# Performance work log

Hardware: AMD Instinct MI355X
Metric: run time of the kernel (lower is better)

## Reference

```python
import jax, jax.numpy as jnp
import numpy as np

B, S, H, E, F, TOP_K = 4, 2048, 512, 16, 1024, 2


def setup_inputs() -> dict:
    key = jax.random.key(0)
    k0, k1, k2, k3, k4 = jax.random.split(key, 5)
    scale = 0.02
    return {
        "inputs": jax.random.normal(k0, (B, S, H), dtype=jnp.float32),
        "router_w": jax.random.normal(k1, (E, H), dtype=jnp.float32) * scale,
        "gate_w": jax.random.normal(k2, (E, H, F), dtype=jnp.float32) * scale,
        "up_w": jax.random.normal(k3, (E, H, F), dtype=jnp.float32) * scale,
        "down_w": jax.random.normal(k4, (E, F, H), dtype=jnp.float32) * scale,
    }


def _moe_forward(inputs, router_w, gate_w, up_w, down_w):
    b, s, h = inputs.shape
    x = inputs.reshape(-1, h)                      # [T, H]
    T = x.shape[0]
    # --- routing: topk of logits then fp32 softmax over the k selected ---
    router_logits = x @ router_w.T                 # [T, E]
    top_vals, top_idx = jax.lax.top_k(router_logits, TOP_K)   # [T, K]
    weights = jax.nn.softmax(top_vals.astype(jnp.float32), axis=-1)  # [T, K]
    # dense combine weights: w[t, e] = routing weight if expert e selected else 0
    combine = jnp.zeros((T, router_w.shape[0]), jnp.float32)
    combine = combine.at[jnp.arange(T)[:, None], top_idx].set(weights)  # [T, E]

    # --- per-expert SwiGLU MLP, weighted combine (scan over experts) ---
    def step(acc, ew):
        wg, wu, wd, ce = ew                        # [H,F], [H,F], [F,H], [T]
        hid = jax.nn.silu(x @ wg) * (x @ wu)       # [T, F]
        y = hid @ wd                               # [T, H]
        return acc + ce[:, None] * y, None

    out0 = jnp.zeros_like(x)
    out, _ = jax.lax.scan(step, out0, (gate_w, up_w, down_w, combine.T))
    return out.reshape(b, s, h), router_logits, top_idx


def reference(inputs, router_w, gate_w, up_w, down_w):
    out, router_logits, selected_experts = _moe_forward(
        inputs, router_w, gate_w, up_w, down_w)
    return out
```

## Files before the change

kernel.cpp:

```cpp
#include <hip/hip_runtime.h>
#include <cstdint>
#include <cstddef>

#define T_TOK 8192
#define H_DIM 512
#define E_NUM 16
#define F_DIM 1024

typedef __bf16 bf16x8 __attribute__((ext_vector_type(8)));
typedef float f32x4 __attribute__((ext_vector_type(4)));

#define OFF_XBF  0UL
#define OFF_HID  8388608UL
#define OFF_GW   41943040UL
#define OFF_UW   58720256UL
#define OFF_DW   75497472UL
#define OFF_STOK 92274688UL
#define OFF_SW   92340224UL
#define OFF_TOPE 92405760UL
#define OFF_TOPW 92471296UL
#define OFF_CNT  92536832UL
#define OFF_CUR  92537856UL
#define OFF_OFFS 92538880UL
#define OFF_SIDX 92539904UL
#define OFF_L128 92605440UL
#define OFF_L64  92606464UL
#define OFF_YB   OFF_GW

__device__ __forceinline__ unsigned short f2bf(float f) {
  union { float f; uint32_t u; } v; v.f = f;
  uint32_t r = v.u + 0x7fffu + ((v.u >> 16) & 1u);
  return (unsigned short)(r >> 16);
}

__device__ __forceinline__ float bf2f(unsigned short u) {
  union { uint32_t u; float f; } v; v.u = (uint32_t)u << 16;
  return v.f;
}

__device__ __forceinline__ void gld16(const void* g, void* l) {
  __builtin_amdgcn_global_load_lds(
      (const __attribute__((address_space(1))) unsigned int*)g,
      (__attribute__((address_space(3))) unsigned int*)l, 16, 0, 0);
}

__global__ __launch_bounds__(256) void k_pre(
    const float* __restrict__ x, const float* __restrict__ rw,
    const float* __restrict__ gw, const float* __restrict__ uw,
    const float* __restrict__ dw,
    unsigned short* __restrict__ xbf, int* __restrict__ tope,
    float* __restrict__ topw,
    unsigned short* __restrict__ gws, unsigned short* __restrict__ uws,
    unsigned short* __restrict__ dws) {
  const int bid = blockIdx.x;
  const int tid = threadIdx.x;
  __shared__ __align__(16) uint32_t lsu[4096];

  if (bid < 3072) {
    const int isgu = (bid < 2048);
    const float* src;
    unsigned short* dst;
    size_t obase0;
    int ldn;
    int e, kc;
    if (isgu) {
      e = bid >> 7;
      const int mat = (bid >> 6) & 1;
      kc = (bid >> 2) & 15;
      const int f2 = bid & 3;
      src = (mat ? uw : gw) + (size_t)e * H_DIM * F_DIM + (size_t)kc * 32 * F_DIM + f2 * 256;
      dst = mat ? uws : gws;
      obase0 = (((size_t)e * 8 + f2 * 2) * 16 + kc) * 4096;
      ldn = F_DIM;
    } else {
      const int r = bid - 2048;
      e = r >> 6;
      kc = (r >> 1) & 31;
      const int ht = r & 1;
      src = dw + (size_t)e * F_DIM * H_DIM + (size_t)kc * 32 * H_DIM + ht * 256;
      dst = dws;
      obase0 = (((size_t)e * 2 + ht) * 32 + kc) * 8192;
      ldn = H_DIM;
    }
    const int nb = tid & 63, kb = tid >> 6;
    const float* s0 = src + (size_t)kb * 8 * ldn + nb * 4;
    float4 v[8];
    #pragma unroll
    for (int j = 0; j < 8; ++j) v[j] = *(const float4*)(s0 + (size_t)j * ldn);
    #pragma unroll
    for (int i = 0; i < 4; ++i) {
      const int n = nb * 4 + i;
      uint4 q;
      q.x = (uint32_t)f2bf(((const float*)&v[0])[i]) | ((uint32_t)f2bf(((const float*)&v[1])[i]) << 16);
      q.y = (uint32_t)f2bf(((const float*)&v[2])[i]) | ((uint32_t)f2bf(((const float*)&v[3])[i]) << 16);
      q.z = (uint32_t)f2bf(((const float*)&v[4])[i]) | ((uint32_t)f2bf(((const float*)&v[5])[i]) << 16);
      q.w = (uint32_t)f2bf(((const float*)&v[6])[i]) | ((uint32_t)f2bf(((const float*)&v[7])[i]) << 16);
      const int jr = n >> 1, sw = (jr ^ (jr >> 3)) & 7;
      const int ccs = (((n & 1) << 2) + kb) ^ sw;
      *(uint4*)&lsu[jr * 32 + ccs * 4] = q;
    }
    __syncthreads();
    const int n = tid;
    const int jr = n >> 1, sw = (jr ^ (jr >> 3)) & 7;
    #pragma unroll
    for (int c = 0; c < 4; ++c) {
      const int ccs = (((n & 1) << 2) + c) ^ sw;
      uint4 q = *(const uint4*)&lsu[jr * 32 + ccs * 4];
      if (isgu) {
        const int fi = n & 127, s = (c ^ fi) & 3;
        const size_t ob = obase0 + (size_t)(n >> 7) * 16 * 4096;
        *(uint4*)&dst[ob + fi * 32 + s * 8] = q;
      } else {
        const int s = (c ^ n) & 3;
        *(uint4*)&dst[obase0 + n * 32 + s * 8] = q;
      }
    }
  } else {
    const int rb = bid - 3072;
    const int wave = tid >> 6, lane = tid & 63;
    const int t = rb * 4 + wave;
    const float4* xr = (const float4*)(x + (size_t)t * H_DIM + lane * 8);
    float4 a = xr[0], b = xr[1];
    float xi[8] = {a.x, a.y, a.z, a.w, b.x, b.y, b.z, b.w};
    uint4 o;
    o.x = (uint32_t)f2bf(xi[0]) | ((uint32_t)f2bf(xi[1]) << 16);
    o.y = (uint32_t)f2bf(xi[2]) | ((uint32_t)f2bf(xi[3]) << 16);
    o.z = (uint32_t)f2bf(xi[4]) | ((uint32_t)f2bf(xi[5]) << 16);
    o.w = (uint32_t)f2bf(xi[6]) | ((uint32_t)f2bf(xi[7]) << 16);
    *(uint4*)(xbf + (size_t)t * H_DIM + lane * 8) = o;
    float acc[E_NUM];
    #pragma unroll
    for (int e = 0; e < E_NUM; ++e) {
      const float4* wr = (const float4*)(rw + e * H_DIM + lane * 8);
      float4 wa = wr[0], wb = wr[1];
      acc[e] = xi[0]*wa.x + xi[1]*wa.y + xi[2]*wa.z + xi[3]*wa.w
             + xi[4]*wb.x + xi[5]*wb.y + xi[6]*wb.z + xi[7]*wb.w;
    }
    #pragma unroll
    for (int off = 1; off < 64; off <<= 1) {
      #pragma unroll
      for (int e = 0; e < E_NUM; ++e) acc[e] += __shfl_xor(acc[e], off);
    }
    if (lane == 0) {
      int e0 = 0; float v0 = acc[0];
      #pragma unroll
      for (int e = 1; e < E_NUM; ++e) if (acc[e] > v0) { v0 = acc[e]; e0 = e; }
      int e1 = -1; float v1 = -3.4e38f;
      #pragma unroll
      for (int e = 0; e < E_NUM; ++e) if (e != e0 && acc[e] > v1) { v1 = acc[e]; e1 = e; }
      float ee = __expf(v1 - v0);
      float inv = 1.0f / (1.0f + ee);
      tope[t*2]   = e0; tope[t*2+1] = e1;
      topw[t*2]   = inv; topw[t*2+1] = ee * inv;
    }
  }
}

__global__ __launch_bounds__(256) void k_hist(
    const int* __restrict__ tope, int* __restrict__ counts) {
  __shared__ int lh[E_NUM];
  const int tid = threadIdx.x;
  if (tid < E_NUM) lh[tid] = 0;
  __syncthreads();
  atomicAdd(&lh[tope[blockIdx.x * 256 + tid]], 1);
  __syncthreads();
  if (tid < E_NUM) atomicAdd(&counts[tid * 16], lh[tid]);
}

__global__ void k_offsets(const int* __restrict__ counts, int* __restrict__ offs,
                          int* __restrict__ list128, int* __restrict__ list64) {
  __shared__ int sc[16], b128[16], b64[16];
  if (threadIdx.x == 0) {
    int s = 0, a = 0, b = 0;
    for (int e = 0; e < E_NUM; ++e) {
      int c = counts[e * 16];
      sc[e] = c; b128[e] = a; b64[e] = b;
      offs[e] = s;
      s += c; a += (c + 127) >> 7; b += (c + 63) >> 6;
    }
    offs[16] = s; offs[18] = a; offs[19] = b;
  }
  __syncthreads();
  for (int e = 0; e < E_NUM; ++e) {
    const int n1 = (sc[e] + 127) >> 7;
    for (int ti = threadIdx.x; ti < n1; ti += 64) list128[b128[e] + ti] = (e << 24) | (ti << 7);
    const int n2 = (sc[e] + 63) >> 6;
    for (int ti = threadIdx.x; ti < n2; ti += 64) list64[b64[e] + ti] = (e << 24) | (ti << 6);
  }
}

__global__ __launch_bounds__(256) void k_scatter(
    const int* __restrict__ tope, const float* __restrict__ topw,
    const int* __restrict__ offs, int* __restrict__ cursors,
    int* __restrict__ stok, float* __restrict__ sw, int* __restrict__ sidx) {
  __shared__ int lh[E_NUM];
  __shared__ int lbase[E_NUM];
  const int tid = threadIdx.x;
  const int t = blockIdx.x * 256 + tid;
  if (tid < E_NUM) lh[tid] = 0;
  __syncthreads();
  int e0 = tope[t*2], e1 = tope[t*2+1];
  int r0 = atomicAdd(&lh[e0], 1);
  int r1 = atomicAdd(&lh[e1], 1);
  __syncthreads();
  if (tid < E_NUM) lbase[tid] = atomicAdd(&cursors[tid * 16], lh[tid]);
  __syncthreads();
  int s0 = offs[e0] + lbase[e0] + r0;
  int s1 = offs[e1] + lbase[e1] + r1;
  stok[s0] = t; sw[s0] = topw[t*2];
  stok[s1] = t; sw[s1] = topw[t*2+1];
  sidx[t*2] = s0; sidx[t*2+1] = s1;
}

__global__ __launch_bounds__(256, 2) void k_gateup(
    const unsigned short* __restrict__ xbf,
    const unsigned short* __restrict__ gws, const unsigned short* __restrict__ uws,
    const int* __restrict__ stok, const int* __restrict__ counts,
    const int* __restrict__ offs, const int* __restrict__ list128,
    unsigned short* __restrict__ hid) {
  const int y = blockIdx.y;
  if (y >= offs[18]) return;
  const int v = list128[y];
  const int e = v >> 24, t0 = v & 0xffffff;
  const int cnt = counts[e * 16];
  const int base = offs[e];
  const int fx = blockIdx.x;

  __shared__ __align__(16) unsigned short sb[2][3][4096];

  const int tid = threadIdx.x;
  const int wave = tid >> 6, lane = tid & 63;
  const int l15 = lane & 15, hi = lane >> 4;
  const int wm = wave >> 1, wn = wave & 1;

  const int r0 = tid >> 2, slot = tid & 3;
  const int rr0 = min(t0 + r0, cnt - 1), rr1 = min(t0 + r0 + 64, cnt - 1);
  const char* sA0 = (const char*)xbf + (size_t)stok[base + rr0] * 1024 + ((slot ^ (r0 & 3)) * 16);
  const char* sA1 = (const char*)xbf + (size_t)stok[base + rr1] * 1024 + ((slot ^ (r0 & 3)) * 16);
  const char* sG = (const char*)gws + (((size_t)e * 8 + fx) * 16) * 8192 + tid * 16;
  const char* sU = (const char*)uws + (((size_t)e * 8 + fx) * 16) * 8192 + tid * 16;
  unsigned short* const dA = &sb[0][0][wave * 512];
  unsigned short* const dG = &sb[0][1][wave * 512];
  unsigned short* const dU = &sb[0][2][wave * 512];
  const int bufo = 3 * 4096;

  f32x4 accg[4][4] = {}; f32x4 accu[4][4] = {};

  #define STAGE_GU(b, kk) { \
    gld16(sA0 + (kk)*64, dA + (b)*bufo); \
    gld16(sA1 + (kk)*64, dA + (b)*bufo + 2048); \
    gld16(sG + (size_t)(kk)*8192, dG + (b)*bufo); \
    gld16(sG + (size_t)(kk)*8192 + 4096, dG + (b)*bufo + 2048); \
    gld16(sU + (size_t)(kk)*8192, dU + (b)*bufo); \
    gld16(sU + (size_t)(kk)*8192 + 4096, dU + (b)*bufo + 2048); }

  STAGE_GU(0, 0);
  __syncthreads();
  #pragma unroll 1
  for (int kk = 0; kk < 16; ++kk) {
    const int cur = kk & 1;
    if (kk < 15) STAGE_GU(cur ^ 1, kk + 1);
    const unsigned short* lA = &sb[cur][0][0];
    const unsigned short* lG = &sb[cur][1][0];
    const unsigned short* lU = &sb[cur][2][0];
    bf16x8 a[4], bg[4], bu[4];
    #pragma unroll
    for (int m = 0; m < 4; ++m) {
      int row = wm*64 + m*16 + l15;
      a[m] = *(const bf16x8*)((const char*)lA + row*64 + (((hi ^ row) & 3) << 4));
    }
    #pragma unroll
    for (int s = 0; s < 4; ++s) {
      int row = wn*64 + s*16 + l15;
      int o = row*64 + (((hi ^ row) & 3) << 4);
      bg[s] = *(const bf16x8*)((const char*)lG + o);
      bu[s] = *(const bf16x8*)((const char*)lU + o);
    }
    #pragma unroll
    for (int m = 0; m < 4; ++m)
      #pragma unroll
      for (int s = 0; s < 4; ++s) {
        accg[m][s] = __builtin_amdgcn_mfma_f32_16x16x32_bf16(a[m], bg[s], accg[m][s], 0, 0, 0);
        accu[m][s] = __builtin_amdgcn_mfma_f32_16x16x32_bf16(a[m], bu[s], accu[m][s], 0, 0, 0);
      }
    __syncthreads();
  }
  #undef STAGE_GU

  #pragma unroll
  for (int m = 0; m < 4; ++m)
    #pragma unroll
    for (int r = 0; r < 4; ++r) {
      int row = t0 + wm*64 + m*16 + hi*4 + r;
      if (row < cnt) {
        #pragma unroll
        for (int s = 0; s < 4; ++s) {
          float g = accg[m][s][r], u = accu[m][s][r];
          float h = g / (1.0f + __expf(-g)) * u;
          hid[(size_t)(base + row) * 1024 + fx*128 + wn*64 + s*16 + l15] = f2bf(h);
        }
      }
    }
}

__global__ __launch_bounds__(256, 3) void k_down(
    const unsigned short* __restrict__ hid, const unsigned short* __restrict__ dws,
    const int* __restrict__ counts, const int* __restrict__ offs,
    const int* __restrict__ list64, unsigned short* __restrict__ ybuf) {
  const int y = blockIdx.y;
  if (y >= offs[19]) return;
  const int v = list64[y];
  const int e = v >> 24, t0 = v & 0xffffff;
  const int cnt = counts[e * 16];
  const int base = offs[e];
  const int ht = blockIdx.x;

  __shared__ __align__(16) unsigned short sbA[2][2048];
  __shared__ __align__(16) unsigned short sbW[2][8192];

  const int tid = threadIdx.x;
  const int wave = tid >> 6, lane = tid & 63;
  const int l15 = lane & 15, hi = lane >> 4;

  const int r0 = tid >> 2, slot = tid & 3;
  const int rr = min(t0 + r0, cnt - 1);
  const char* sA = (const char*)hid + (size_t)(base + rr) * 2048 + ((slot ^ (r0 & 3)) * 16);
  const char* sW = (const char*)dws + (((size_t)e * 2 + ht) * 32) * 16384 + tid * 16;
  unsigned short* const dA = &sbA[0][wave * 512];
  unsigned short* const dW = &sbW[0][wave * 512];

  f32x4 acc[4][4] = {};

  #define STAGE_DN(b, kk) { \
    gld16(sA + (kk)*64, dA + (b)*2048); \
    const char* w = sW + (size_t)(kk)*16384; \
    gld16(w,         dW + (b)*8192); \
    gld16(w + 4096,  dW + (b)*8192 + 2048); \
    gld16(w + 8192,  dW + (b)*8192 + 4096); \
    gld16(w + 12288, dW + (b)*8192 + 6144); }

  STAGE_DN(0, 0);
  __syncthreads();
  #pragma unroll 1
  for (int kk = 0; kk < 32; ++kk) {
    const int cur = kk & 1;
    if (kk < 31) STAGE_DN(cur ^ 1, kk + 1);
    const unsigned short* lA = &sbA[cur][0];
    const unsigned short* lW = &sbW[cur][0];
    bf16x8 a[4], b[4];
    #pragma unroll
    for (int m = 0; m < 4; ++m) {
      int row = m*16 + l15;
      a[m] = *(const bf16x8*)((const char*)lA + row*64 + (((hi ^ row) & 3) << 4));
    }
    #pragma unroll
    for (int s = 0; s < 4; ++s) {
      int row = wave*64 + s*16 + l15;
      b[s] = *(const bf16x8*)((const char*)lW + row*64 + (((hi ^ row) & 3) << 4));
    }
    #pragma unroll
    for (int m = 0; m < 4; ++m)
      #pragma unroll
      for (int s = 0; s < 4; ++s)
        acc[m][s] = __builtin_amdgcn_mfma_f32_16x16x32_bf16(a[m], b[s], acc[m][s], 0, 0, 0);
    __syncthreads();
  }
  #undef STAGE_DN

  #pragma unroll
  for (int m = 0; m < 4; ++m)
    #pragma unroll
    for (int r = 0; r < 4; ++r) {
      int row = t0 + m*16 + hi*4 + r;
      if (row < cnt) {
        unsigned short* yy = ybuf + (size_t)(base + row) * 512 + ht*256 + wave*64;
        #pragma unroll
        for (int s = 0; s < 4; ++s)
          yy[s*16 + l15] = f2bf(acc[m][s][r]);
      }
    }
}

__global__ __launch_bounds__(256) void k_gather(
    const unsigned short* __restrict__ ybuf, const int* __restrict__ sidx,
    const float* __restrict__ topw, float* __restrict__ out) {
  const int wave = threadIdx.x >> 6, lane = threadIdx.x & 63;
  const int t = blockIdx.x * 4 + wave;
  const int s0 = sidx[t*2], s1 = sidx[t*2+1];
  const float w0 = topw[t*2], w1 = topw[t*2+1];
  uint4 a = *(const uint4*)(ybuf + (size_t)s0 * 512 + lane * 8);
  uint4 b = *(const uint4*)(ybuf + (size_t)s1 * 512 + lane * 8);
  float4 o0, o1;
  o0.x = w0*bf2f((unsigned short)(a.x)) + w1*bf2f((unsigned short)(b.x));
  o0.y = w0*bf2f((unsigned short)(a.x>>16)) + w1*bf2f((unsigned short)(b.x>>16));
  o0.z = w0*bf2f((unsigned short)(a.y)) + w1*bf2f((unsigned short)(b.y));
  o0.w = w0*bf2f((unsigned short)(a.y>>16)) + w1*bf2f((unsigned short)(b.y>>16));
  o1.x = w0*bf2f((unsigned short)(a.z)) + w1*bf2f((unsigned short)(b.z));
  o1.y = w0*bf2f((unsigned short)(a.z>>16)) + w1*bf2f((unsigned short)(b.z>>16));
  o1.z = w0*bf2f((unsigned short)(a.w)) + w1*bf2f((unsigned short)(b.w));
  o1.w = w0*bf2f((unsigned short)(a.w>>16)) + w1*bf2f((unsigned short)(b.w>>16));
  float* orow = out + (size_t)t * H_DIM + lane * 8;
  *(float4*)orow = o0;
  *(float4*)(orow + 4) = o1;
}

extern "C" void kernel_launch(void* const* d_in, const int* in_sizes, int n_in,
                              void* d_out, int out_size, void* d_ws, size_t ws_size,
                              hipStream_t stream) {
  const float* x  = (const float*)d_in[0];
  const float* rw = (const float*)d_in[1];
  const float* gw = (const float*)d_in[2];
  const float* uw = (const float*)d_in[3];
  const float* dw = (const float*)d_in[4];
  float* out = (float*)d_out;
  char* ws = (char*)d_ws;

  unsigned short* xbf = (unsigned short*)(ws + OFF_XBF);
  unsigned short* hid = (unsigned short*)(ws + OFF_HID);
  unsigned short* gws = (unsigned short*)(ws + OFF_GW);
  unsigned short* uws = (unsigned short*)(ws + OFF_UW);
  unsigned short* dws = (unsigned short*)(ws + OFF_DW);
  unsigned short* ybuf = (unsigned short*)(ws + OFF_YB);
  int*   stok    = (int*)(ws + OFF_STOK);
  float* swt     = (float*)(ws + OFF_SW);
  int*   tope    = (int*)(ws + OFF_TOPE);
  float* topw    = (float*)(ws + OFF_TOPW);
  int*   counts  = (int*)(ws + OFF_CNT);
  int*   cursors = (int*)(ws + OFF_CUR);
  int*   offs    = (int*)(ws + OFF_OFFS);
  int*   sidx    = (int*)(ws + OFF_SIDX);
  int*   list128 = (int*)(ws + OFF_L128);
  int*   list64  = (int*)(ws + OFF_L64);

  hipMemsetAsync(ws + OFF_CNT, 0, 2048 + 128, stream);

  k_pre<<<5120, 256, 0, stream>>>(x, rw, gw, uw, dw, xbf, tope, topw, gws, uws, dws);
  k_hist<<<T_TOK * 2 / 256, 256, 0, stream>>>(tope, counts);
  k_offsets<<<1, 64, 0, stream>>>(counts, offs, list128, list64);
  k_scatter<<<T_TOK / 256, 256, 0, stream>>>(tope, topw, offs, cursors, stok, swt, sidx);
  k_gateup<<<dim3(8, 160), 256, 0, stream>>>(
      xbf, gws, uws, stok, counts, offs, list128, hid);
  k_down<<<dim3(2, 288), 256, 0, stream>>>(
      hid, dws, counts, offs, list64, ybuf);
  k_gather<<<T_TOK / 4, 256, 0, stream>>>(ybuf, sidx, topw, out);
}
```

Before: 153.9 us.

## Fuse histogram into prep, move down-weight conversion into gate/up kernel, drop LDS transpose

The expert histogram is now computed inside the routing blocks of the prep kernel, which removes the separate k_hist launch. The fp32-to-bf16 conversion of the down-projection weights moves out of the prep kernel and into 1024 extra blocks appended to the gate/up launch. Those blocks can then overlap with the gate/up GEMM instead of sitting on the critical path before routing. The weight repack now writes straight to global memory in the swizzled layout and skips the LDS transpose round-trip, which may make the global stores less coalesced. The extra blocks also compete with the GEMM blocks for compute units.

```diff
diff --git a/kernel.cpp b/kernel.cpp
--- a/kernel.cpp
+++ b/kernel.cpp
@@ -44,79 +44,47 @@
       (__attribute__((address_space(3))) unsigned int*)l, 16, 0, 0);
 }
 
+__device__ __forceinline__ uint4 pack8(const float4 v[8], int i) {
+  uint4 q;
+  q.x = (uint32_t)f2bf(((const float*)&v[0])[i]) | ((uint32_t)f2bf(((const float*)&v[1])[i]) << 16);
+  q.y = (uint32_t)f2bf(((const float*)&v[2])[i]) | ((uint32_t)f2bf(((const float*)&v[3])[i]) << 16);
+  q.z = (uint32_t)f2bf(((const float*)&v[4])[i]) | ((uint32_t)f2bf(((const float*)&v[5])[i]) << 16);
+  q.w = (uint32_t)f2bf(((const float*)&v[6])[i]) | ((uint32_t)f2bf(((const float*)&v[7])[i]) << 16);
+  return q;
+}
+
 __global__ __launch_bounds__(256) void k_pre(
     const float* __restrict__ x, const float* __restrict__ rw,
     const float* __restrict__ gw, const float* __restrict__ uw,
-    const float* __restrict__ dw,
     unsigned short* __restrict__ xbf, int* __restrict__ tope,
     float* __restrict__ topw,
     unsigned short* __restrict__ gws, unsigned short* __restrict__ uws,
-    unsigned short* __restrict__ dws) {
+    int* __restrict__ counts) {
   const int bid = blockIdx.x;
   const int tid = threadIdx.x;
-  __shared__ __align__(16) uint32_t lsu[4096];
-
-  if (bid < 3072) {
-    const int isgu = (bid < 2048);
-    const float* src;
-    unsigned short* dst;
-    size_t obase0;
-    int ldn;
-    int e, kc;
-    if (isgu) {
-      e = bid >> 7;
-      const int mat = (bid >> 6) & 1;
-      kc = (bid >> 2) & 15;
-      const int f2 = bid & 3;
-      src = (mat ? uw : gw) + (size_t)e * H_DIM * F_DIM + (size_t)kc * 32 * F_DIM + f2 * 256;
-      dst = mat ? uws : gws;
-      obase0 = (((size_t)e * 8 + f2 * 2) * 16 + kc) * 4096;
-      ldn = F_DIM;
-    } else {
-      const int r = bid - 2048;
-      e = r >> 6;
-      kc = (r >> 1) & 31;
-      const int ht = r & 1;
-      src = dw + (size_t)e * F_DIM * H_DIM + (size_t)kc * 32 * H_DIM + ht * 256;
-      dst = dws;
-      obase0 = (((size_t)e * 2 + ht) * 32 + kc) * 8192;
-      ldn = H_DIM;
-    }
+  __shared__ int lh[E_NUM];
+
+  if (bid < 2048) {
+    const int e = bid >> 7, mat = (bid >> 6) & 1, kc = (bid >> 2) & 15, f2 = bid & 3;
+    const float* src = (mat ? uw : gw) + (size_t)e * H_DIM * F_DIM
+                     + (size_t)kc * 32 * F_DIM + f2 * 256;
+    unsigned short* dst = mat ? uws : gws;
     const int nb = tid & 63, kb = tid >> 6;
-    const float* s0 = src + (size_t)kb * 8 * ldn + nb * 4;
+    const float* s0 = src + (size_t)kb * 8 * F_DIM + nb * 4;
     float4 v[8];
     #pragma unroll
-    for (int j = 0; j < 8; ++j) v[j] = *(const float4*)(s0 + (size_t)j * ldn);
+    for (int j = 0; j < 8; ++j) v[j] = *(const float4*)(s0 + (size_t)j * F_DIM);
     #pragma unroll
     for (int i = 0; i < 4; ++i) {
-      const int n = nb * 4 + i;
-      uint4 q;
-      q.x = (uint32_t)f2bf(((const float*)&v[0])[i]) | ((uint32_t)f2bf(((const float*)&v[1])[i]) << 16);
-      q.y = (uint32_t)f2bf(((const float*)&v[2])[i]) | ((uint32_t)f2bf(((const float*)&v[3])[i]) << 16);
-      q.z = (uint32_t)f2bf(((const float*)&v[4])[i]) | ((uint32_t)f2bf(((const float*)&v[5])[i]) << 16);
-      q.w = (uint32_t)f2bf(((const float*)&v[6])[i]) | ((uint32_t)f2bf(((const float*)&v[7])[i]) << 16);
-      const int jr = n >> 1, sw = (jr ^ (jr >> 3)) & 7;
-      const int ccs = (((n & 1) << 2) + kb) ^ sw;
-      *(uint4*)&lsu[jr * 32 + ccs * 4] = q;
-    }
+      const int nl = nb * 4 + i;
+      const int fx = f2 * 2 + (nl >> 7), fi = nl & 127;
+      const size_t ob = (((size_t)e * 8 + fx) * 16 + kc) * 4096;
+      *(uint4*)&dst[ob + fi * 32 + ((kb ^ fi) & 3) * 8] = pack8(v, i);
+    }
+  } else {
+    if (tid < E_NUM) lh[tid] = 0;
     __syncthreads();
-    const int n = tid;
-    const int jr = n >> 1, sw = (jr ^ (jr >> 3)) & 7;
-    #pragma unroll
-    for (int c = 0; c < 4; ++c) {
-      const int ccs = (((n & 1) << 2) + c) ^ sw;
-      uint4 q = *(const uint4*)&lsu[jr * 32 + ccs * 4];
-      if (isgu) {
-        const int fi = n & 127, s = (c ^ fi) & 3;
-        const size_t ob = obase0 + (size_t)(n >> 7) * 16 * 4096;
-        *(uint4*)&dst[ob + fi * 32 + s * 8] = q;
-      } else {
-        const int s = (c ^ n) & 3;
-        *(uint4*)&dst[obase0 + n * 32 + s * 8] = q;
-      }
-    }
-  } else {
-    const int rb = bid - 3072;
+    const int rb = bid - 2048;
     const int wave = tid >> 6, lane = tid & 63;
     const int t = rb * 4 + wave;
     const float4* xr = (const float4*)(x + (size_t)t * H_DIM + lane * 8);
@@ -152,19 +120,12 @@
       float inv = 1.0f / (1.0f + ee);
       tope[t*2]   = e0; tope[t*2+1] = e1;
       topw[t*2]   = inv; topw[t*2+1] = ee * inv;
-    }
-  }
-}
-
-__global__ __launch_bounds__(256) void k_hist(
-    const int* __restrict__ tope, int* __restrict__ counts) {
-  __shared__ int lh[E_NUM];
-  const int tid = threadIdx.x;
-  if (tid < E_NUM) lh[tid] = 0;
-  __syncthreads();
-  atomicAdd(&lh[tope[blockIdx.x * 256 + tid]], 1);
-  __syncthreads();
-  if (tid < E_NUM) atomicAdd(&counts[tid * 16], lh[tid]);
+      atomicAdd(&lh[e0], 1);
+      atomicAdd(&lh[e1], 1);
+    }
+    __syncthreads();
+    if (tid < E_NUM && lh[tid] > 0) atomicAdd(&counts[tid * 16], lh[tid]);
+  }
 }
 
 __global__ void k_offsets(const int* __restrict__ counts, int* __restrict__ offs,
@@ -217,8 +178,29 @@
     const unsigned short* __restrict__ gws, const unsigned short* __restrict__ uws,
     const int* __restrict__ stok, const int* __restrict__ counts,
     const int* __restrict__ offs, const int* __restrict__ list128,
-    unsigned short* __restrict__ hid) {
+    unsigned short* __restrict__ hid,
+    const float* __restrict__ dwf, unsigned short* __restrict__ dws) {
   const int y = blockIdx.y;
+  const int tid = threadIdx.x;
+
+  if (y >= 160) {
+    const int u = (y - 160) * 8 + blockIdx.x;
+    const int e = u >> 6, kc = (u >> 1) & 31, ht = u & 1;
+    const float* src = dwf + (size_t)e * F_DIM * H_DIM
+                     + (size_t)kc * 32 * H_DIM + ht * 256;
+    const int nb = tid & 63, kb = tid >> 6;
+    const float* s0 = src + (size_t)kb * 8 * H_DIM + nb * 4;
+    float4 v[8];
+    #pragma unroll
+    for (int j = 0; j < 8; ++j) v[j] = *(const float4*)(s0 + (size_t)j * H_DIM);
+    const size_t ob = (((size_t)e * 2 + ht) * 32 + kc) * 8192;
+    #pragma unroll
+    for (int i = 0; i < 4; ++i) {
+      const int n = nb * 4 + i;
+      *(uint4*)&dws[ob + n * 32 + ((kb ^ n) & 3) * 8] = pack8(v, i);
+    }
+    return;
+  }
   if (y >= offs[18]) return;
   const int v = list128[y];
   const int e = v >> 24, t0 = v & 0xffffff;
@@ -228,7 +210,6 @@
 
   __shared__ __align__(16) unsigned short sb[2][3][4096];
 
-  const int tid = threadIdx.x;
   const int wave = tid >> 6, lane = tid & 63;
   const int l15 = lane & 15, hi = lane >> 4;
   const int wm = wave >> 1, wn = wave & 1;
@@ -434,12 +415,11 @@
 
   hipMemsetAsync(ws + OFF_CNT, 0, 2048 + 128, stream);
 
-  k_pre<<<5120, 256, 0, stream>>>(x, rw, gw, uw, dw, xbf, tope, topw, gws, uws, dws);
-  k_hist<<<T_TOK * 2 / 256, 256, 0, stream>>>(tope, counts);
+  k_pre<<<4096, 256, 0, stream>>>(x, rw, gw, uw, xbf, tope, topw, gws, uws, counts);
   k_offsets<<<1, 64, 0, stream>>>(counts, offs, list128, list64);
   k_scatter<<<T_TOK / 256, 256, 0, stream>>>(tope, topw, offs, cursors, stok, swt, sidx);
-  k_gateup<<<dim3(8, 160), 256, 0, stream>>>(
-      xbf, gws, uws, stok, counts, offs, list128, hid);
+  k_gateup<<<dim3(8, 288), 256, 0, stream>>>(
+      xbf, gws, uws, stok, counts, offs, list128, hid, dw, dws);
   k_down<<<dim3(2, 288), 256, 0, stream>>>(
       hid, dws, counts, offs, list64, ybuf);
   k_gather<<<T_TOK / 4, 256, 0, stream>>>(ybuf, sidx, topw, out);
```

Measured after the change: 157.3 us. 2.2% more time.
